# Kernel tuning notes

Measured on AMD Instinct MI355X. Metric: run time of the kernel, lower is better.

The kernel has to match this reference:

```python
import jax, jax.numpy as jnp
import numpy as np

B, D, H, O, E, K = 8192, 1024, 4096, 1024, 8, 2

def setup_inputs() -> dict:
    key = jax.random.key(0)
    ks = jax.random.split(key, 8)
    x = jax.random.normal(ks[0], (B, D), dtype=jnp.float32)
    topk_idx = jax.random.randint(ks[1], (B, K), 0, E, dtype=jnp.int32)
    weights = jax.random.uniform(ks[2], (B, K), dtype=jnp.float32)
    s1 = 1.0 / np.sqrt(D)
    s2 = 1.0 / np.sqrt(H)
    W1 = jax.random.uniform(ks[3], (E, D, H), minval=-s1, maxval=s1, dtype=jnp.float32)
    b1 = jax.random.uniform(ks[4], (E, H), minval=-s1, maxval=s1, dtype=jnp.float32)
    W2 = jax.random.uniform(ks[5], (E, H, O), minval=-s2, maxval=s2, dtype=jnp.float32)
    b2 = jax.random.uniform(ks[6], (E, O), minval=-s2, maxval=s2, dtype=jnp.float32)
    return {"x": x, "topk_idx": topk_idx, "weights": weights,
            "W1": W1, "b1": b1, "W2": W2, "b2": b2}

def reference(x, topk_idx, weights, W1, b1, W2, b2):
    # Per-token gate mass for each expert: gate[b,e] = sum_i weights[b,i]*[topk_idx[b,i]==e]
    # Equivalent to the original masked gather/scatter combine (duplicates in topk_idx sum).
    out = jnp.zeros((x.shape[0], W2.shape[-1]), dtype=x.dtype)
    for e in range(W1.shape[0]):  # small fixed loop over experts
        gate_e = jnp.sum(weights * (topk_idx == e), axis=1)  # [B]
        h = jax.nn.relu(x @ W1[e] + b1[e])                   # [B,H]
        out_e = h @ W2[e] + b2[e]                            # [B,O]
        out = out + gate_e[:, None] * out_e
    return out
```

## Files before the change

### kernel.cpp

```cpp
#include <hip/hip_runtime.h>
#include <stdint.h>

#define B_TOK 8192
#define D_DIM 1024
#define H_DIM 4096
#define O_DIM 1024
#define E_NUM 8
#define K_TOP 2
#define NPAIR (B_TOK * K_TOP)

typedef short bf16x8 __attribute__((ext_vector_type(8)));
typedef float f32x4 __attribute__((ext_vector_type(4)));

struct Hdr {
    int counts[8];
    int offsets[9];
    int total1, total2;
    int base1[9];
    int base2[9];
};

__device__ __forceinline__ unsigned short f2bf(float f) {
    union { float f; unsigned int u; } v; v.f = f;
    unsigned int u = v.u;
    unsigned int r = (u + 0x7fffu + ((u >> 16) & 1u)) >> 16;
    return (unsigned short)r;
}

__device__ __forceinline__ float bf2f(unsigned short s) {
    union { unsigned int u; float f; } v;
    v.u = ((unsigned int)s) << 16;
    return v.f;
}

__device__ __forceinline__ void async16(const void* g, const void* l) {
    __builtin_amdgcn_global_load_lds(
        (__attribute__((address_space(1))) void*)(uintptr_t)g,
        (__attribute__((address_space(3))) void*)(uint32_t)(uintptr_t)l,
        16, 0, 0);
}


__global__ void cvt_x_kernel(const float* __restrict__ x, unsigned short* __restrict__ xb) {
    int i = (blockIdx.x * 256 + threadIdx.x) * 4;
    float4 v = *(const float4*)(x + i);
    ushort4 o;
    o.x = f2bf(v.x); o.y = f2bf(v.y); o.z = f2bf(v.z); o.w = f2bf(v.w);
    *(ushort4*)(xb + i) = o;
}

__global__ __launch_bounds__(256) void tconv_kernel(const float* __restrict__ in,
                                                    unsigned short* __restrict__ out,
                                                    int R, int C) {
    __shared__ float t[64 * 69];
    int e = blockIdx.z;
    const float* ip = in + (size_t)e * R * C;
    unsigned short* op = out + (size_t)e * R * C;
    int c0 = blockIdx.x * 64, r0 = blockIdx.y * 64;
    int tid = threadIdx.x;
    int lr = tid >> 4;
    int lc = (tid & 15) * 4;
#pragma unroll
    for (int i = 0; i < 4; i++) {
        int row = lr + i * 16;
        float4 v = *(const float4*)&ip[(size_t)(r0 + row) * C + c0 + lc];
        t[row * 69 + lc + 0] = v.x;
        t[row * 69 + lc + 1] = v.y;
        t[row * 69 + lc + 2] = v.z;
        t[row * 69 + lc + 3] = v.w;
    }
    __syncthreads();
#pragma unroll
    for (int i = 0; i < 4; i++) {
        int c = lr + i * 16;
        ushort4 o;
        o.x = f2bf(t[(lc + 0) * 69 + c]);
        o.y = f2bf(t[(lc + 1) * 69 + c]);
        o.z = f2bf(t[(lc + 2) * 69 + c]);
        o.w = f2bf(t[(lc + 3) * 69 + c]);
        *(ushort4*)&op[(size_t)(c0 + c) * R + r0 + lc] = o;
    }
}


__global__ __launch_bounds__(1024) void route_kernel(const int* __restrict__ topk,
                                                     Hdr* hdr,
                                                     int* __restrict__ ptok,
                                                     int* __restrict__ pslot) {
    __shared__ int cnt[8];
    __shared__ int cur[8];
    int tid = threadIdx.x;
    if (tid < 8) cnt[tid] = 0;
    __syncthreads();
    int ev[16];
#pragma unroll
    for (int j = 0; j < 16; j++) {
        ev[j] = topk[tid + j * 1024];
        atomicAdd(&cnt[ev[j]], 1);
    }
    __syncthreads();
    if (tid == 0) {
        int off = 0, t1 = 0, t2 = 0;
        for (int e = 0; e < 8; e++) {
            int c = cnt[e];
            hdr->counts[e] = c;
            hdr->offsets[e] = off;
            cur[e] = off;
            hdr->base1[e] = t1;
            hdr->base2[e] = t2;
            int mt = (c + 255) >> 8;
            t1 += mt * (H_DIM / 256);
            t2 += mt * (O_DIM / 128);
            off += c;
        }
        hdr->offsets[8] = off;
        hdr->base1[8] = t1;
        hdr->base2[8] = t2;
        hdr->total1 = t1;
        hdr->total2 = t2;
    }
    __syncthreads();
#pragma unroll
    for (int j = 0; j < 16; j++) {
        int i = tid + j * 1024;
        int pos = atomicAdd(&cur[ev[j]], 1);
        ptok[pos] = i >> 1;
        pslot[i] = pos;
    }
}

__global__ void ws_fail_kernel(float* out) { out[0] = 1.0e9f; }


#define ASL(BUF, KH) ((BUF) * 32768 + (KH) * 16384)

#define STG_A(BUF, KH, KOFF) do { \
    async16(Ab + srcA[0] + (KOFF), smem + ASL(BUF, KH) + wu * 2048); \
    async16(Ab + srcA[1] + (KOFF), smem + ASL(BUF, KH) + wu * 2048 + 1024); } while (0)

#define STG_B(BUF, KH, KOFF) do { \
    async16(Bb + srcB[0] + (KOFF), smem + 65536 + ASL(BUF, KH) + wu * 2048); \
    async16(Bb + srcB[1] + (KOFF), smem + 65536 + ASL(BUF, KH) + wu * 2048 + 1024); } while (0)

#define VM6 asm volatile("s_waitcnt vmcnt(6)" ::: "memory")
#define VM4 asm volatile("s_waitcnt vmcnt(4)" ::: "memory")
#define VM0 asm volatile("s_waitcnt vmcnt(0)" ::: "memory")
#define NOPX ((void)0)

#define PHASE0(BUF, KH, STAGE, CKPT) do { \
    STAGE; \
    bq[0] = *(const bf16x8*)&smem[pBo[0] + ASL(BUF, KH)]; \
    bq[1] = *(const bf16x8*)&smem[pBo[1] + ASL(BUF, KH)]; \
    bq[2] = *(const bf16x8*)&smem[pBo[2] + ASL(BUF, KH)]; \
    bq[3] = *(const bf16x8*)&smem[pBo[3] + ASL(BUF, KH)]; \
    aq[0] = *(const bf16x8*)&smem[pAo[0] + ASL(BUF, KH)]; \
    aq[1] = *(const bf16x8*)&smem[pAo[1] + ASL(BUF, KH)]; \
    aq[2] = *(const bf16x8*)&smem[pAo[2] + ASL(BUF, KH)]; \
    aq[3] = *(const bf16x8*)&smem[pAo[3] + ASL(BUF, KH)]; \
    __builtin_amdgcn_s_barrier(); \
    asm volatile("s_waitcnt lgkmcnt(0)" ::: "memory"); \
    __builtin_amdgcn_s_setprio(1); \
    _Pragma("unroll") \
    for (int q_ = 0; q_ < 4; ++q_) { \
        _Pragma("unroll") \
        for (int n_ = 0; n_ < 4; ++n_) \
            acc[q_][n_] = __builtin_amdgcn_mfma_f32_16x16x32_bf16(aq[q_], bq[n_], acc[q_][n_], 0, 0, 0); \
    } \
    __builtin_amdgcn_s_setprio(0); \
    CKPT; \
    __builtin_amdgcn_s_barrier(); \
} while (0)

#define PHASE1(BUF, KH, STAGE, CKPT) do { \
    STAGE; \
    aq[0] = *(const bf16x8*)&smem[pAo[4] + ASL(BUF, KH)]; \
    aq[1] = *(const bf16x8*)&smem[pAo[5] + ASL(BUF, KH)]; \
    aq[2] = *(const bf16x8*)&smem[pAo[6] + ASL(BUF, KH)]; \
    aq[3] = *(const bf16x8*)&smem[pAo[7] + ASL(BUF, KH)]; \
    __builtin_amdgcn_s_barrier(); \
    asm volatile("s_waitcnt lgkmcnt(0)" ::: "memory"); \
    __builtin_amdgcn_s_setprio(1); \
    _Pragma("unroll") \
    for (int q_ = 0; q_ < 4; ++q_) { \
        _Pragma("unroll") \
        for (int n_ = 0; n_ < 4; ++n_) \
            acc[4 + q_][n_] = __builtin_amdgcn_mfma_f32_16x16x32_bf16(aq[q_], bq[n_], acc[4 + q_][n_], 0, 0, 0); \
    } \
    __builtin_amdgcn_s_setprio(0); \
    CKPT; \
    __builtin_amdgcn_s_barrier(); \
} while (0)

template <int KD, int N, bool GATHER>
__global__ __launch_bounds__(512, 2) void moe_gemm256_kernel(
    const unsigned short* __restrict__ A,
    const unsigned short* __restrict__ Bt,
    const float* __restrict__ bias,
    const Hdr* __restrict__ hdr,
    const int* __restrict__ ptok,
    unsigned short* __restrict__ outp) {

    extern __shared__ __align__(16) char smem[];
    constexpr int NT = KD / 64;
    constexpr int NI = NT / 2;
    static_assert(NT >= 4 && (NT % 2) == 0, "K-tile count");

    const int tid = threadIdx.x;
    const int lane = tid & 63;
    const int wv = tid >> 6;
    const int wu = __builtin_amdgcn_readfirstlane(wv);
    const int lr = lane & 15;
    const int lkg = lane >> 4;
    const int wr = wv >> 2;
    const int wc = wv & 3;

    const int total = hdr->total1;
    const int* tb = hdr->base1;

    int chunk = (total + 7) >> 3;
    int seq = (blockIdx.x & 7) * chunk + (blockIdx.x >> 3);
    if (seq >= total) return;

    int e = 0;
#pragma unroll
    for (int j = 1; j < 8; j++)
        if (seq >= tb[j]) e = j;
    e = __builtin_amdgcn_readfirstlane(e);
    int lt = seq - tb[e];
    int cnt = hdr->counts[e], off = hdr->offsets[e];
    int MT = (cnt + 255) >> 8;
    int mtile = lt % MT, ntile = lt / MT;
    int m0 = mtile * 256, n0 = ntile * 256;

    const char* Ab = (const char*)A;
    const char* Bb = (const char*)(Bt + (size_t)e * ((size_t)N * KD));

    uint32_t srcA[2], srcB[2];
#pragma unroll
    for (int l = 0; l < 2; ++l) {
        int g = wv * 128 + l * 64 + lane;
        int rp = g >> 2, cp = g & 3;
        int c = (cp - (rp >> 1)) & 3;
        int q = off + m0 + rp;
        q = q > NPAIR - 1 ? NPAIR - 1 : q;
        uint32_t rowA = GATHER ? (uint32_t)ptok[q] : (uint32_t)q;
        srcA[l] = rowA * (uint32_t)(KD * 2) + (uint32_t)(c * 16);
        srcB[l] = (uint32_t)(n0 + rp) * (uint32_t)(KD * 2) + (uint32_t)(c * 16);
    }

    uint32_t pAo[8], pBo[4];
#pragma unroll
    for (int mr = 0; mr < 8; ++mr) {
        int r = wr * 128 + mr * 16 + lr;
        pAo[mr] = (uint32_t)(r * 64 + ((lkg + (r >> 1)) & 3) * 16);
    }
#pragma unroll
    for (int nr = 0; nr < 4; ++nr) {
        int r = wc * 64 + nr * 16 + lr;
        pBo[nr] = (uint32_t)(65536 + r * 64 + ((lkg + (r >> 1)) & 3) * 16);
    }

    f32x4 acc[8][4];
#pragma unroll
    for (int i = 0; i < 8; ++i)
#pragma unroll
        for (int j = 0; j < 4; ++j)
            acc[i][j] = (f32x4){0.f, 0.f, 0.f, 0.f};
    bf16x8 aq[4], bq[4];

    STG_A(0, 0, 0u);   STG_B(0, 0, 0u);
    STG_A(0, 1, 64u);  STG_B(0, 1, 64u);
    STG_A(1, 0, 128u); STG_B(1, 0, 128u);
    STG_B(1, 1, 192u);
    VM0;
    __builtin_amdgcn_s_barrier();

    for (int it = 0; it < NI - 1; ++it) {
        const uint32_t kb = (uint32_t)it * 256u;
        PHASE0(0, 0, STG_A(1, 1, kb + 192u), NOPX);
        PHASE1(0, 0, STG_B(0, 0, kb + 256u), NOPX);
        PHASE0(0, 1, STG_A(0, 0, kb + 256u), NOPX);
        PHASE1(0, 1, STG_B(0, 1, kb + 320u), VM6);
        PHASE0(1, 0, STG_A(0, 1, kb + 320u), NOPX);
        PHASE1(1, 0, STG_B(1, 0, kb + 384u), NOPX);
        PHASE0(1, 1, STG_A(1, 0, kb + 384u), NOPX);
        PHASE1(1, 1, STG_B(1, 1, kb + 448u), VM6);
    }
    {
        const uint32_t kb = (uint32_t)(NI - 1) * 256u;
        PHASE0(0, 0, STG_A(1, 1, kb + 192u), NOPX);
        PHASE1(0, 0, NOPX, NOPX);
        PHASE0(0, 1, NOPX, NOPX);
        PHASE1(0, 1, NOPX, VM0);
        PHASE0(1, 0, NOPX, NOPX);
        PHASE1(1, 0, NOPX, NOPX);
        PHASE0(1, 1, NOPX, NOPX);
        PHASE1(1, 1, NOPX, NOPX);
    }

    unsigned short* eb = (unsigned short*)smem;
    int rows_valid = cnt - m0;
    if (rows_valid > 256) rows_valid = 256;
#pragma unroll
    for (int pass = 0; pass < 2; ++pass) {
        __syncthreads();
        if (wr == pass) {
#pragma unroll
            for (int nr = 0; nr < 4; ++nr) {
                int n = wc * 64 + nr * 16 + lr;
                float bv = bias[(size_t)e * N + n0 + n];
#pragma unroll
                for (int mr = 0; mr < 8; ++mr) {
#pragma unroll
                    for (int r2 = 0; r2 < 4; ++r2) {
                        int ml = mr * 16 + lkg * 4 + r2;
                        float v = acc[mr][nr][r2] + bv;
                        if (GATHER) v = v > 0.f ? v : 0.f;
                        eb[ml * 264 + n] = f2bf(v);
                    }
                }
            }
        }
        __syncthreads();
        int rv = rows_valid - pass * 128;
        if (rv > 128) rv = 128;
#pragma unroll
        for (int j = 0; j < 8; ++j) {
            int idx = j * 512 + tid;
            int row = idx >> 5;
            int c16 = idx & 31;
            if (row < rv) {
                uint4 v = *(const uint4*)&eb[row * 264 + c16 * 8];
                *(uint4*)&outp[(size_t)(off + m0 + pass * 128 + row) * N + n0 + c16 * 8] = v;
            }
        }
    }
}


#define BSL(BUF, KH) (65536 + (BUF) * 16384 + (KH) * 8192)

#define STG2B(BUF, KH, KOFF) \
    async16(Bb + srcB + (KOFF), smem + BSL(BUF, KH) + wu * 1024)

#define G2PH0(BUF, KH, STAGE, CKPT) do { \
    STAGE; \
    bq[0] = *(const bf16x8*)&smem[pBo[0] + BSL(BUF, KH)]; \
    bq[1] = *(const bf16x8*)&smem[pBo[1] + BSL(BUF, KH)]; \
    aq[0] = *(const bf16x8*)&smem[pAo[0] + ASL(BUF, KH)]; \
    aq[1] = *(const bf16x8*)&smem[pAo[1] + ASL(BUF, KH)]; \
    aq[2] = *(const bf16x8*)&smem[pAo[2] + ASL(BUF, KH)]; \
    aq[3] = *(const bf16x8*)&smem[pAo[3] + ASL(BUF, KH)]; \
    __builtin_amdgcn_s_barrier(); \
    asm volatile("s_waitcnt lgkmcnt(0)" ::: "memory"); \
    __builtin_amdgcn_s_setprio(1); \
    _Pragma("unroll") \
    for (int q_ = 0; q_ < 4; ++q_) { \
        _Pragma("unroll") \
        for (int n_ = 0; n_ < 2; ++n_) \
            acc[q_][n_] = __builtin_amdgcn_mfma_f32_16x16x32_bf16(aq[q_], bq[n_], acc[q_][n_], 0, 0, 0); \
    } \
    __builtin_amdgcn_s_setprio(0); \
    CKPT; \
    __builtin_amdgcn_s_barrier(); \
} while (0)

#define G2PH1(BUF, KH, STAGE, CKPT) do { \
    STAGE; \
    aq[0] = *(const bf16x8*)&smem[pAo[4] + ASL(BUF, KH)]; \
    aq[1] = *(const bf16x8*)&smem[pAo[5] + ASL(BUF, KH)]; \
    aq[2] = *(const bf16x8*)&smem[pAo[6] + ASL(BUF, KH)]; \
    aq[3] = *(const bf16x8*)&smem[pAo[7] + ASL(BUF, KH)]; \
    __builtin_amdgcn_s_barrier(); \
    asm volatile("s_waitcnt lgkmcnt(0)" ::: "memory"); \
    __builtin_amdgcn_s_setprio(1); \
    _Pragma("unroll") \
    for (int q_ = 0; q_ < 4; ++q_) { \
        _Pragma("unroll") \
        for (int n_ = 0; n_ < 2; ++n_) \
            acc[4 + q_][n_] = __builtin_amdgcn_mfma_f32_16x16x32_bf16(aq[q_], bq[n_], acc[4 + q_][n_], 0, 0, 0); \
    } \
    __builtin_amdgcn_s_setprio(0); \
    CKPT; \
    __builtin_amdgcn_s_barrier(); \
} while (0)

template <int KD, int N>
__global__ __launch_bounds__(512, 2) void moe_gemm2_kernel(
    const unsigned short* __restrict__ A,
    const unsigned short* __restrict__ Bt,
    const float* __restrict__ bias,
    const Hdr* __restrict__ hdr,
    unsigned short* __restrict__ outp) {

    extern __shared__ __align__(16) char smem[];
    constexpr int NT = KD / 64;
    constexpr int NI = NT / 2;
    static_assert(NT >= 4 && (NT % 2) == 0, "K-tile count");

    const int tid = threadIdx.x;
    const int lane = tid & 63;
    const int wv = tid >> 6;
    const int wu = __builtin_amdgcn_readfirstlane(wv);
    const int lr = lane & 15;
    const int lkg = lane >> 4;
    const int wr = wv >> 2;
    const int wc = wv & 3;

    const int total = hdr->total2;
    const int* tb = hdr->base2;

    int chunk = (total + 7) >> 3;
    int seq = (blockIdx.x & 7) * chunk + (blockIdx.x >> 3);
    if (seq >= total) return;

    int e = 0;
#pragma unroll
    for (int j = 1; j < 8; j++)
        if (seq >= tb[j]) e = j;
    e = __builtin_amdgcn_readfirstlane(e);
    int lt = seq - tb[e];
    int cnt = hdr->counts[e], off = hdr->offsets[e];
    int MT = (cnt + 255) >> 8;
    int mtile = lt % MT, ntile = lt / MT;
    int m0 = mtile * 256, n0 = ntile * 128;

    const char* Ab = (const char*)A;
    const char* Bb = (const char*)(Bt + (size_t)e * ((size_t)N * KD));

    uint32_t srcA[2];
#pragma unroll
    for (int l = 0; l < 2; ++l) {
        int g = wv * 128 + l * 64 + lane;
        int rp = g >> 2, cp = g & 3;
        int c = (cp - (rp >> 1)) & 3;
        int q = off + m0 + rp;
        q = q > NPAIR - 1 ? NPAIR - 1 : q;
        srcA[l] = (uint32_t)q * (uint32_t)(KD * 2) + (uint32_t)(c * 16);
    }
    uint32_t srcB;
    {
        int g = wv * 64 + lane;
        int rp = g >> 2, cp = g & 3;
        int c = (cp - (rp >> 1)) & 3;
        srcB = (uint32_t)(n0 + rp) * (uint32_t)(KD * 2) + (uint32_t)(c * 16);
    }

    uint32_t pAo[8], pBo[2];
#pragma unroll
    for (int mr = 0; mr < 8; ++mr) {
        int r = wr * 128 + mr * 16 + lr;
        pAo[mr] = (uint32_t)(r * 64 + ((lkg + (r >> 1)) & 3) * 16);
    }
#pragma unroll
    for (int nr = 0; nr < 2; ++nr) {
        int r = wc * 32 + nr * 16 + lr;
        pBo[nr] = (uint32_t)(r * 64 + ((lkg + (r >> 1)) & 3) * 16);
    }

    f32x4 acc[8][2];
#pragma unroll
    for (int i = 0; i < 8; ++i)
#pragma unroll
        for (int j = 0; j < 2; ++j)
            acc[i][j] = (f32x4){0.f, 0.f, 0.f, 0.f};
    bf16x8 aq[4], bq[2];

    STG_A(0, 0, 0u);   STG2B(0, 0, 0u);
    STG_A(0, 1, 64u);  STG2B(0, 1, 64u);
    STG_A(1, 0, 128u); STG2B(1, 0, 128u);
    STG2B(1, 1, 192u);
    VM0;
    __builtin_amdgcn_s_barrier();

    for (int it = 0; it < NI - 1; ++it) {
        const uint32_t kb = (uint32_t)it * 256u;
        G2PH0(0, 0, STG_A(1, 1, kb + 192u), NOPX);
        G2PH1(0, 0, STG2B(0, 0, kb + 256u), NOPX);
        G2PH0(0, 1, STG_A(0, 0, kb + 256u), NOPX);
        G2PH1(0, 1, STG2B(0, 1, kb + 320u), VM4);
        G2PH0(1, 0, STG_A(0, 1, kb + 320u), NOPX);
        G2PH1(1, 0, STG2B(1, 0, kb + 384u), NOPX);
        G2PH0(1, 1, STG_A(1, 0, kb + 384u), NOPX);
        G2PH1(1, 1, STG2B(1, 1, kb + 448u), VM4);
    }
    {
        const uint32_t kb = (uint32_t)(NI - 1) * 256u;
        G2PH0(0, 0, STG_A(1, 1, kb + 192u), NOPX);
        G2PH1(0, 0, NOPX, NOPX);
        G2PH0(0, 1, NOPX, NOPX);
        G2PH1(0, 1, NOPX, VM0);
        G2PH0(1, 0, NOPX, NOPX);
        G2PH1(1, 0, NOPX, NOPX);
        G2PH0(1, 1, NOPX, NOPX);
        G2PH1(1, 1, NOPX, NOPX);
    }

    unsigned short* eb = (unsigned short*)smem;
    int rows_valid = cnt - m0;
    if (rows_valid > 256) rows_valid = 256;
#pragma unroll
    for (int pass = 0; pass < 2; ++pass) {
        __syncthreads();
        if (wr == pass) {
#pragma unroll
            for (int nr = 0; nr < 2; ++nr) {
                int n = wc * 32 + nr * 16 + lr;
                float bv = bias[(size_t)e * N + n0 + n];
#pragma unroll
                for (int mr = 0; mr < 8; ++mr) {
#pragma unroll
                    for (int r2 = 0; r2 < 4; ++r2) {
                        int ml = mr * 16 + lkg * 4 + r2;
                        eb[ml * 132 + n] = f2bf(acc[mr][nr][r2] + bv);
                    }
                }
            }
        }
        __syncthreads();
        int rv = rows_valid - pass * 128;
        if (rv > 128) rv = 128;
#pragma unroll
        for (int j = 0; j < 8; ++j) {
            int idx = j * 512 + tid;
            int row = idx >> 5;
            int lc8 = idx & 31;
            if (row < rv) {
                uint2 v = *(const uint2*)&eb[row * 132 + lc8 * 4];
                *(uint2*)&outp[(size_t)(off + m0 + pass * 128 + row) * N + n0 + lc8 * 4] = v;
            }
        }
    }
}

__global__ void combine_kernel(const unsigned short* __restrict__ oslot,
                               const int* __restrict__ pslot,
                               const float* __restrict__ wts,
                               float* __restrict__ out) {
    int tok = blockIdx.x;
    int s0 = pslot[tok * 2], s1 = pslot[tok * 2 + 1];
    float g0 = wts[tok * 2], g1 = wts[tok * 2 + 1];
    int n = threadIdx.x * 4;
    ushort4 a = *(const ushort4*)&oslot[(size_t)s0 * O_DIM + n];
    ushort4 b = *(const ushort4*)&oslot[(size_t)s1 * O_DIM + n];
    float4 o;
    o.x = g0 * bf2f(a.x) + g1 * bf2f(b.x);
    o.y = g0 * bf2f(a.y) + g1 * bf2f(b.y);
    o.z = g0 * bf2f(a.z) + g1 * bf2f(b.z);
    o.w = g0 * bf2f(a.w) + g1 * bf2f(b.w);
    *(float4*)&out[(size_t)tok * O_DIM + n] = o;
}


extern "C" void kernel_launch(void* const* d_in, const int* in_sizes, int n_in,
                              void* d_out, int out_size, void* d_ws, size_t ws_size,
                              hipStream_t stream) {
    const float* x   = (const float*)d_in[0];
    const int* topk  = (const int*)d_in[1];
    const float* wts = (const float*)d_in[2];
    const float* W1  = (const float*)d_in[3];
    const float* b1  = (const float*)d_in[4];
    const float* W2  = (const float*)d_in[5];
    const float* b2  = (const float*)d_in[6];
    float* out = (float*)d_out;

    char* ws = (char*)d_ws;
    size_t off = 0;
    auto alloc = [&](size_t bytes) -> void* {
        void* p = ws + off;
        off += (bytes + 255) & ~(size_t)255;
        return p;
    };
    Hdr* hdr = (Hdr*)alloc(sizeof(Hdr));
    int* ptok = (int*)alloc((size_t)NPAIR * 4);
    int* pslot = (int*)alloc((size_t)NPAIR * 4);
    unsigned short* xb   = (unsigned short*)alloc((size_t)B_TOK * D_DIM * 2);
    unsigned short* W1bt = (unsigned short*)alloc((size_t)E_NUM * D_DIM * H_DIM * 2);
    unsigned short* W2bt = (unsigned short*)alloc((size_t)E_NUM * H_DIM * O_DIM * 2);
    unsigned short* hbuf = (unsigned short*)alloc((size_t)NPAIR * H_DIM * 2);
    unsigned short* oslot = W1bt;

    if (off > ws_size) {
        hipMemsetAsync(d_out, 0, (size_t)out_size * sizeof(float), stream);
        ws_fail_kernel<<<1, 1, 0, stream>>>(out);
        return;
    }

    static int attr_done = 0;
    if (!attr_done) {
        (void)hipFuncSetAttribute(
            reinterpret_cast<const void*>(&moe_gemm256_kernel<D_DIM, H_DIM, true>),
            hipFuncAttributeMaxDynamicSharedMemorySize, 131072);
        (void)hipFuncSetAttribute(
            reinterpret_cast<const void*>(&moe_gemm2_kernel<H_DIM, O_DIM>),
            hipFuncAttributeMaxDynamicSharedMemorySize, 98304);
        attr_done = 1;
    }

    cvt_x_kernel<<<(B_TOK * D_DIM) / 1024, 256, 0, stream>>>(x, xb);
    tconv_kernel<<<dim3(H_DIM / 64, D_DIM / 64, E_NUM), dim3(256), 0, stream>>>(W1, W1bt, D_DIM, H_DIM);
    tconv_kernel<<<dim3(O_DIM / 64, H_DIM / 64, E_NUM), dim3(256), 0, stream>>>(W2, W2bt, H_DIM, O_DIM);
    route_kernel<<<1, 1024, 0, stream>>>(topk, hdr, ptok, pslot);

    moe_gemm256_kernel<D_DIM, H_DIM, true><<<1152, 512, 131072, stream>>>(
        xb, W1bt, b1, hdr, ptok, hbuf);
    moe_gemm2_kernel<H_DIM, O_DIM><<<576, 512, 98304, stream>>>(
        hbuf, W2bt, b2, hdr, oslot);
    combine_kernel<<<B_TOK, 256, 0, stream>>>(oslot, pslot, wts, out);
}
```

Baseline: 735.8 us.

## Merge gemm2 half-phases into one phase per K-slice with fused A/B staging

Collapses the two half-phases per K-slice in the second MoE GEMM into a single phase. Each phase now loads all eight A fragments and both B fragments, issues 16 MFMAs, and stages the matching A and B slices together. This halves the number of barrier pairs per K-tile and re-times the async prefetch (the vmcnt wait becomes 3, and the prologue no longer preloads the last B slice). In exchange it holds more fragment registers, which could hurt occupancy under the 2-waves bound, and it shortens the prefetch distance for B.

```diff
diff --git a/kernel.cpp b/kernel.cpp
--- a/kernel.cpp
+++ b/kernel.cpp
@@ -143,7 +143,7 @@
     async16(Bb + srcB[1] + (KOFF), smem + 65536 + ASL(BUF, KH) + wu * 2048 + 1024); } while (0)
 
 #define VM6 asm volatile("s_waitcnt vmcnt(6)" ::: "memory")
-#define VM4 asm volatile("s_waitcnt vmcnt(4)" ::: "memory")
+#define VM3 asm volatile("s_waitcnt vmcnt(3)" ::: "memory")
 #define VM0 asm volatile("s_waitcnt vmcnt(0)" ::: "memory")
 #define NOPX ((void)0)
 
@@ -343,19 +343,24 @@
 #define STG2B(BUF, KH, KOFF) \
     async16(Bb + srcB + (KOFF), smem + BSL(BUF, KH) + wu * 1024)
 
-#define G2PH0(BUF, KH, STAGE, CKPT) do { \
-    STAGE; \
+#define G2PH(BUF, KH, SA, SB, CKPT) do { \
+    SA; \
+    SB; \
     bq[0] = *(const bf16x8*)&smem[pBo[0] + BSL(BUF, KH)]; \
     bq[1] = *(const bf16x8*)&smem[pBo[1] + BSL(BUF, KH)]; \
     aq[0] = *(const bf16x8*)&smem[pAo[0] + ASL(BUF, KH)]; \
     aq[1] = *(const bf16x8*)&smem[pAo[1] + ASL(BUF, KH)]; \
     aq[2] = *(const bf16x8*)&smem[pAo[2] + ASL(BUF, KH)]; \
     aq[3] = *(const bf16x8*)&smem[pAo[3] + ASL(BUF, KH)]; \
+    aq[4] = *(const bf16x8*)&smem[pAo[4] + ASL(BUF, KH)]; \
+    aq[5] = *(const bf16x8*)&smem[pAo[5] + ASL(BUF, KH)]; \
+    aq[6] = *(const bf16x8*)&smem[pAo[6] + ASL(BUF, KH)]; \
+    aq[7] = *(const bf16x8*)&smem[pAo[7] + ASL(BUF, KH)]; \
     __builtin_amdgcn_s_barrier(); \
     asm volatile("s_waitcnt lgkmcnt(0)" ::: "memory"); \
     __builtin_amdgcn_s_setprio(1); \
     _Pragma("unroll") \
-    for (int q_ = 0; q_ < 4; ++q_) { \
+    for (int q_ = 0; q_ < 8; ++q_) { \
         _Pragma("unroll") \
         for (int n_ = 0; n_ < 2; ++n_) \
             acc[q_][n_] = __builtin_amdgcn_mfma_f32_16x16x32_bf16(aq[q_], bq[n_], acc[q_][n_], 0, 0, 0); \
@@ -365,26 +370,6 @@
     __builtin_amdgcn_s_barrier(); \
 } while (0)
 
-#define G2PH1(BUF, KH, STAGE, CKPT) do { \
-    STAGE; \
-    aq[0] = *(const bf16x8*)&smem[pAo[4] + ASL(BUF, KH)]; \
-    aq[1] = *(const bf16x8*)&smem[pAo[5] + ASL(BUF, KH)]; \
-    aq[2] = *(const bf16x8*)&smem[pAo[6] + ASL(BUF, KH)]; \
-    aq[3] = *(const bf16x8*)&smem[pAo[7] + ASL(BUF, KH)]; \
-    __builtin_amdgcn_s_barrier(); \
-    asm volatile("s_waitcnt lgkmcnt(0)" ::: "memory"); \
-    __builtin_amdgcn_s_setprio(1); \
-    _Pragma("unroll") \
-    for (int q_ = 0; q_ < 4; ++q_) { \
-        _Pragma("unroll") \
-        for (int n_ = 0; n_ < 2; ++n_) \
-            acc[4 + q_][n_] = __builtin_amdgcn_mfma_f32_16x16x32_bf16(aq[q_], bq[n_], acc[4 + q_][n_], 0, 0, 0); \
-    } \
-    __builtin_amdgcn_s_setprio(0); \
-    CKPT; \
-    __builtin_amdgcn_s_barrier(); \
-} while (0)
-
 template <int KD, int N>
 __global__ __launch_bounds__(512, 2) void moe_gemm2_kernel(
     const unsigned short* __restrict__ A,
@@ -464,36 +449,27 @@
 #pragma unroll
         for (int j = 0; j < 2; ++j)
             acc[i][j] = (f32x4){0.f, 0.f, 0.f, 0.f};
-    bf16x8 aq[4], bq[2];
+    bf16x8 aq[8], bq[2];
 
     STG_A(0, 0, 0u);   STG2B(0, 0, 0u);
     STG_A(0, 1, 64u);  STG2B(0, 1, 64u);
     STG_A(1, 0, 128u); STG2B(1, 0, 128u);
-    STG2B(1, 1, 192u);
     VM0;
     __builtin_amdgcn_s_barrier();
 
     for (int it = 0; it < NI - 1; ++it) {
         const uint32_t kb = (uint32_t)it * 256u;
-        G2PH0(0, 0, STG_A(1, 1, kb + 192u), NOPX);
-        G2PH1(0, 0, STG2B(0, 0, kb + 256u), NOPX);
-        G2PH0(0, 1, STG_A(0, 0, kb + 256u), NOPX);
-        G2PH1(0, 1, STG2B(0, 1, kb + 320u), VM4);
-        G2PH0(1, 0, STG_A(0, 1, kb + 320u), NOPX);
-        G2PH1(1, 0, STG2B(1, 0, kb + 384u), NOPX);
-        G2PH0(1, 1, STG_A(1, 0, kb + 384u), NOPX);
-        G2PH1(1, 1, STG2B(1, 1, kb + 448u), VM4);
+        G2PH(0, 0, STG_A(1, 1, kb + 192u), STG2B(1, 1, kb + 192u), NOPX);
+        G2PH(0, 1, STG_A(0, 0, kb + 256u), STG2B(0, 0, kb + 256u), VM3);
+        G2PH(1, 0, STG_A(0, 1, kb + 320u), STG2B(0, 1, kb + 320u), NOPX);
+        G2PH(1, 1, STG_A(1, 0, kb + 384u), STG2B(1, 0, kb + 384u), VM3);
     }
     {
         const uint32_t kb = (uint32_t)(NI - 1) * 256u;
-        G2PH0(0, 0, STG_A(1, 1, kb + 192u), NOPX);
-        G2PH1(0, 0, NOPX, NOPX);
-        G2PH0(0, 1, NOPX, NOPX);
-        G2PH1(0, 1, NOPX, VM0);
-        G2PH0(1, 0, NOPX, NOPX);
-        G2PH1(1, 0, NOPX, NOPX);
-        G2PH0(1, 1, NOPX, NOPX);
-        G2PH1(1, 1, NOPX, NOPX);
+        G2PH(0, 0, STG_A(1, 1, kb + 192u), STG2B(1, 1, kb + 192u), NOPX);
+        G2PH(0, 1, NOPX, NOPX, VM0);
+        G2PH(1, 0, NOPX, NOPX, NOPX);
+        G2PH(1, 1, NOPX, NOPX, NOPX);
     }
 
     unsigned short* eb = (unsigned short*)smem;
```

After: 743.7 us. No clear change (+1.1%).
